# Optimization experiments

Hardware: AMD Instinct MI355X
Metric: run time of the kernel (lower is better)

Reference implementation:

```python
import jax, jax.numpy as jnp
import numpy as np

B, T, DM, H, DK, N_STEPS = 4, 1024, 1024, 16, 64, 3


def setup_inputs() -> dict:
    key = jax.random.key(0)
    ks = jax.random.split(key, 8)
    s = 1.0 / np.sqrt(DM).astype(np.float32)
    x = jax.random.normal(ks[0], (B, T, DM), jnp.float32)
    W_Q = jax.random.normal(ks[1], (DM, DM), jnp.float32) * s
    W_K = jax.random.normal(ks[2], (DM, DM), jnp.float32) * s
    W_re = jax.random.normal(ks[3], (DM, DM), jnp.float32) * s
    W_im = jax.random.normal(ks[4], (DM, DM), jnp.float32) * s
    W_V = jax.random.normal(ks[5], (DM, DM), jnp.float32) * s
    W_O = jax.random.normal(ks[6], (DM, DM), jnp.float32) * s
    logit_lam = jnp.float32(0.0)  # sigmoid(0)=0.5 == cfg.lam
    return {"x": x, "W_Q": W_Q, "W_K": W_K, "W_re": W_re, "W_im": W_im,
            "W_V": W_V, "W_O": W_O, "logit_lam": logit_lam}


def _heads(y):
    # (B,T,DM) -> (B,H,T,DK)
    return y.reshape(B, T, H, DK).transpose(0, 2, 1, 3)


def reference(x, W_Q, W_K, W_re, W_im, W_V, W_O, logit_lam):
    # AdjacencyBuilder: soft row-normalized adjacency
    Q = _heads(x @ W_Q)
    K = _heads(x @ W_K)
    scores = jnp.einsum('bhtd,bhsd->bhts', Q, K) / jnp.float32(np.sqrt(DK))
    A = jax.nn.softmax(scores, axis=-1)                      # (B,H,T,T)
    # PhaseEncoding: complex oscillator versors
    D = jax.lax.complex(_heads(x @ W_re), _heads(x @ W_im))  # (B,H,T,DK) c64
    # TopologyPropagation: D <- (1-lam) D + lam A D, n_steps times
    lam = jax.nn.sigmoid(logit_lam)
    A_c = A.astype(jnp.complex64)
    for _ in range(N_STEPS):
        D = (1.0 - lam) * D + lam * jnp.einsum('bhts,bhsd->bhtd', A_c, D)
    # CollapseReadout (phase_align): softmax over T of cosine to mean field
    mean_D = jnp.mean(D, axis=-2, keepdims=True)             # (B,H,1,DK)
    dot = (D * jnp.conj(mean_D)).real
    norm = jnp.abs(D) * jnp.abs(mean_D) + 1e-8
    gate = jax.nn.softmax(dot / norm, axis=-2)               # (B,H,T,DK)
    # Value gating + output projection (dropout is identity in eval)
    V = _heads(x @ W_V)
    out = (gate * V).transpose(0, 2, 1, 3).reshape(B, T, DM) @ W_O
    return out, gate
```

## Files before the change

kernel.cpp:

```cpp
#include <hip/hip_runtime.h>
#include <math.h>

#define Bc 4
#define Tc 1024
#define DMc 1024
#define Hc 16
#define DKc 64
#define BHc 64
#define Mc 4096
#define TD (Tc*DKc)
#define TD2 (Tc*128)
#define TDS (128*2048)

typedef __bf16 bf16_t;
typedef bf16_t bf16x4 __attribute__((ext_vector_type(4)));
typedef bf16_t bf16x8 __attribute__((ext_vector_type(8)));
typedef float  f32x4  __attribute__((ext_vector_type(4)));

#define KLSTR 136
#define DLSTR 72

__device__ __forceinline__ bf16x8 ld8(const bf16_t* p) {
    return *(const bf16x8*)p;
}
__device__ __forceinline__ void packsplit4(bf16_t* dh, bf16_t* dl, float4 v) {
    bf16x4 h, l;
    h[0]=(bf16_t)v.x; l[0]=(bf16_t)(v.x-(float)h[0]);
    h[1]=(bf16_t)v.y; l[1]=(bf16_t)(v.y-(float)h[1]);
    h[2]=(bf16_t)v.z; l[2]=(bf16_t)(v.z-(float)h[2]);
    h[3]=(bf16_t)v.w; l[3]=(bf16_t)(v.w-(float)h[3]);
    *(bf16x4*)dh = h; *(bf16x4*)dl = l;
}
__device__ __forceinline__ unsigned pk2(bf16_t a, bf16_t b) {
    unsigned short ua = __builtin_bit_cast(unsigned short, a);
    unsigned short ub = __builtin_bit_cast(unsigned short, b);
    return (unsigned)ua | ((unsigned)ub << 16);
}
__device__ __forceinline__ void gload16(const bf16_t* g, bf16_t* l) {
    __builtin_amdgcn_global_load_lds(
        (__attribute__((address_space(1))) void*)(bf16_t*)g,
        (__attribute__((address_space(3))) void*)l, 16, 0, 0);
}

__global__ __launch_bounds__(256)
void convx_k(const float* __restrict__ x,
             bf16_t* __restrict__ xh, bf16_t* __restrict__ xl)
{
    size_t i = ((size_t)blockIdx.x * 256 + threadIdx.x) * 4;
    float4 v = *(const float4*)&x[i];
    packsplit4(&xh[i], &xl[i], v);
}

__global__ __launch_bounds__(256)
void convw_k(const float* __restrict__ W0, const float* __restrict__ W1,
             const float* __restrict__ W2, const float* __restrict__ W3,
             const float* __restrict__ W4, const float* __restrict__ W5,
             bf16_t* __restrict__ WT)
{
    __shared__ float tile[32][33];
    const float* Ws[6] = {W0, W1, W2, W3, W4, W5};
    const int wi = blockIdx.z;
    const float* W = Ws[wi];
    bf16_t* WTh = WT + (size_t)wi * 2097152;
    bf16_t* WTl = WTh + 1048576;

    const int tx = threadIdx.x & 31, ty = threadIdx.x >> 5;
    const int k0 = blockIdx.x * 32, n0 = blockIdx.y * 32;
#pragma unroll
    for (int i = 0; i < 4; i++)
        tile[ty + 8*i][tx] = W[(size_t)(k0 + ty + 8*i) * DMc + n0 + tx];
    __syncthreads();
    const int kg = threadIdx.x & 7, n = threadIdx.x >> 3;
    float4 v = make_float4(tile[kg*4+0][n], tile[kg*4+1][n],
                           tile[kg*4+2][n], tile[kg*4+3][n]);
    const size_t o = (size_t)(n0 + n) * DMc + k0 + kg*4;
    packsplit4(&WTh[o], &WTl[o], v);
}

template<int MODE>
__global__ __launch_bounds__(256)
void mgemm_k(const bf16_t* __restrict__ Ah, const bf16_t* __restrict__ Al,
             const bf16_t* __restrict__ WT,
             bf16_t* __restrict__ Oq, bf16_t* __restrict__ Ok,
             bf16_t* __restrict__ Od, float* __restrict__ Ov,
             float* __restrict__ Of)
{
    __shared__ bf16_t S[4][128*32];

    const int tid = threadIdx.x;
    const int wv  = tid >> 6;
    const int ln  = tid & 63;
    const int l15 = ln & 15;
    const int qd  = ln >> 4;
    const int m0  = blockIdx.x * 128;
    const int by  = blockIdx.y;

    const bf16_t *Bh, *Bl;
    int n0, sel, kt0, kt1;
    float* Opart;
    if (MODE == 0) {
        sel = by >> 3;
        n0 = (by & 7) * 128;
        Bh = WT + (size_t)sel * 2097152;
        Bl = Bh + 1048576;
        kt0 = 0; kt1 = DMc;
        Opart = nullptr;
    } else {
        sel = 5;
        Bh = WT + (size_t)5 * 2097152;
        Bl = Bh + 1048576;
        n0 = by * 128;
        kt0 = blockIdx.z * 512; kt1 = kt0 + 512;
        Opart = Of + (size_t)blockIdx.z * ((size_t)Mc * DMc);
    }

    const int srow = ln >> 2;
    const int scol = (ln & 3) * 8;
    const bf16_t* sbase;
    if (wv == 0)      sbase = Ah + (size_t)(m0 + srow) * DMc + scol;
    else if (wv == 1) sbase = Al + (size_t)(m0 + srow) * DMc + scol;
    else if (wv == 2) sbase = Bh + (size_t)(n0 + srow) * DMc + scol;
    else              sbase = Bl + (size_t)(n0 + srow) * DMc + scol;
    sbase += kt0;
    bf16_t* ldst = &S[wv][0];

    f32x4 acc[4][4];
#pragma unroll
    for (int i = 0; i < 4; i++)
#pragma unroll
        for (int j = 0; j < 4; j++) acc[i][j] = (f32x4)0.f;

#pragma unroll 1
    for (int kt = kt0; kt < kt1; kt += 32) {
        __syncthreads();
#pragma unroll
        for (int i = 0; i < 8; i++)
            gload16(sbase + (size_t)i * 16 * DMc, ldst + i * 512);
        sbase += 32;
        __syncthreads();

        bf16x8 fah[4], fal[4], fbh[4], fbl[4];
#pragma unroll
        for (int it = 0; it < 4; it++) {
            const int row = ((wv>>1)*64 + it*16 + l15) * 32 + qd*8;
            fah[it] = *(const bf16x8*)&S[0][row];
            fal[it] = *(const bf16x8*)&S[1][row];
        }
#pragma unroll
        for (int jt = 0; jt < 4; jt++) {
            const int row = ((wv&1)*64 + jt*16 + l15) * 32 + qd*8;
            fbh[jt] = *(const bf16x8*)&S[2][row];
            fbl[jt] = *(const bf16x8*)&S[3][row];
        }
#pragma unroll
        for (int it = 0; it < 4; it++)
#pragma unroll
            for (int jt = 0; jt < 4; jt++) {
                acc[it][jt] = __builtin_amdgcn_mfma_f32_16x16x32_bf16(
                    fah[it], fbh[jt], acc[it][jt], 0, 0, 0);
                acc[it][jt] = __builtin_amdgcn_mfma_f32_16x16x32_bf16(
                    fah[it], fbl[jt], acc[it][jt], 0, 0, 0);
                acc[it][jt] = __builtin_amdgcn_mfma_f32_16x16x32_bf16(
                    fal[it], fbh[jt], acc[it][jt], 0, 0, 0);
            }
    }

#pragma unroll
    for (int it = 0; it < 4; it++) {
        const int mb = m0 + (wv>>1)*64 + it*16 + qd*4;
#pragma unroll
        for (int jt = 0; jt < 4; jt++) {
            const int col = n0 + (wv&1)*64 + jt*16 + l15;
            if (MODE == 0) {
                const int hh = col >> 6;
                const int b  = mb >> 10, t0 = mb & 1023;
                if (sel <= 1) {
                    bf16_t* O = sel ? Ok : Oq;
                    const int d = col & 63;
#pragma unroll
                    for (int r = 0; r < 4; r++) {
                        const float val = acc[it][jt][r];
                        const size_t o = ((size_t)(b*Hc + hh)*Tc + t0 + r)*128 + d;
                        bf16_t vh = (bf16_t)val;
                        O[o]      = vh;
                        O[o + 64] = (bf16_t)(val - (float)vh);
                    }
                } else if (sel <= 3) {
                    const int d = (sel == 3 ? 64 : 0) + (col & 63);
                    bf16x4 h4, l4;
#pragma unroll
                    for (int r = 0; r < 4; r++) {
                        const float val = acc[it][jt][r];
                        h4[r] = (bf16_t)val;
                        l4[r] = (bf16_t)(val - (float)h4[r]);
                    }
                    const size_t o = (size_t)(b*Hc + hh)*TDS + (size_t)d*2048 + t0;
                    *(bf16x4*)&Od[o]        = h4;
                    *(bf16x4*)&Od[o + 1024] = l4;
                } else {
#pragma unroll
                    for (int r = 0; r < 4; r++)
                        Ov[((size_t)(b*Hc + hh)*Tc + t0 + r)*64 + (col & 63)]
                            = acc[it][jt][r];
                }
            } else {
#pragma unroll
                for (int r = 0; r < 4; r++)
                    Opart[(size_t)(mb + r) * DMc + col] = acc[it][jt][r];
            }
        }
    }
}

__global__ __launch_bounds__(256)
void reduce2_k(const float* __restrict__ p0, const float* __restrict__ p1,
               float* __restrict__ out)
{
    size_t i = ((size_t)blockIdx.x * 256 + threadIdx.x) * 4;
    float4 a = *(const float4*)&p0[i];
    float4 b = *(const float4*)&p1[i];
    *(float4*)&out[i] = make_float4(a.x+b.x, a.y+b.y, a.z+b.z, a.w+b.w);
}

template<int FINAL>
__global__ __launch_bounds__(256)
void prop_k(const bf16_t* __restrict__ Qg, const bf16_t* __restrict__ Kg,
            const bf16_t* __restrict__ DTin, bf16_t* __restrict__ DTout,
            float* __restrict__ Dc, const float* __restrict__ llam)
{
    __shared__ bf16_t Ks[32*KLSTR];
    __shared__ bf16_t Ds[128*DLSTR];

    const int tid = threadIdx.x;
    const int wv  = tid >> 6;
    const int ln  = tid & 63;
    const int l15 = ln & 15;
    const int qd  = ln >> 4;
    const int bh  = blockIdx.x;
    const int Tw  = blockIdx.y * 128 + wv * 32;

    const bf16_t* Qh  = Qg   + (size_t)bh * (Tc*128);
    const bf16_t* Kh  = Kg   + (size_t)bh * (Tc*128);
    const bf16_t* DTh = DTin + (size_t)bh * TDS;

    bf16x8 qfh[2][2], qfl[2][2];
#pragma unroll
    for (int tj = 0; tj < 2; tj++) {
        const bf16_t* qp = &Qh[(size_t)(Tw + tj*16 + l15) * 128];
#pragma unroll
        for (int ks = 0; ks < 2; ks++) {
            qfh[tj][ks] = *(const bf16x8*)&qp[ks*32 + qd*8];
            qfl[tj][ks] = *(const bf16x8*)&qp[64 + ks*32 + qd*8];
        }
    }

    const int idk0 = tid, idk1 = tid + 256;
    const bf16_t* srcK0 = Kh + (size_t)(idk0 >> 4) * 128 + (idk0 & 15) * 8;
    const bf16_t* srcK1 = Kh + (size_t)(idk1 >> 4) * 128 + (idk1 & 15) * 8;
    bf16_t* dstK0 = &Ks[(idk0 >> 4) * KLSTR + (idk0 & 15) * 8];
    bf16_t* dstK1 = &Ks[(idk1 >> 4) * KLSTR + (idk1 & 15) * 8];
    const bf16_t* srcD[4];
    bf16_t* dstD[4];
#pragma unroll
    for (int i = 0; i < 4; i++) {
        const int id = tid + i * 256;
        const int r = id >> 3, sg = id & 7;
        srcD[i] = DTh + (size_t)r * 2048
                      + (sg < 4 ? sg * 8 : 1024 + (sg - 4) * 8);
        dstD[i] = (sg < 4) ? &Ds[r * DLSTR + sg * 8]
                           : &Ds[r * DLSTR + 32 + (sg - 4) * 8];
    }
    bf16x8 kr0 = *(const bf16x8*)srcK0;
    bf16x8 kr1 = *(const bf16x8*)srcK1;
    bf16x8 dr[4];
#pragma unroll
    for (int i = 0; i < 4; i++) dr[i] = *(const bf16x8*)srcD[i];

    f32x4 acc[8][2];
#pragma unroll
    for (int i = 0; i < 8; i++)
#pragma unroll
        for (int j = 0; j < 2; j++) acc[i][j] = (f32x4)0.f;
    float rs[2] = {0.f, 0.f};

    const int srcA = (((qd & 1) * 2)     << 4) | l15;
    const int srcB = (((qd & 1) * 2 + 1) << 4) | l15;
    const bool loQuad = (qd < 2);

#pragma unroll 1
    for (int ch = 0; ch < 32; ch++) {
        __syncthreads();
        *(bf16x8*)dstK0 = kr0;
        *(bf16x8*)dstK1 = kr1;
#pragma unroll
        for (int i = 0; i < 4; i++) *(bf16x8*)dstD[i] = dr[i];
        __syncthreads();
        if (ch < 31) {
            kr0 = *(const bf16x8*)(srcK0 + (size_t)(ch + 1) * 4096);
            kr1 = *(const bf16x8*)(srcK1 + (size_t)(ch + 1) * 4096);
#pragma unroll
            for (int i = 0; i < 4; i++)
                dr[i] = *(const bf16x8*)(srcD[i] + (size_t)(ch + 1) * 32);
        }
        bf16x8 kfh[2][2], kfl[2][2];
#pragma unroll
        for (int si = 0; si < 2; si++) {
            const int row = (si*16 + l15) * KLSTR;
#pragma unroll
            for (int ks = 0; ks < 2; ks++) {
                kfh[si][ks] = ld8(&Ks[row + ks*32 + qd*8]);
                kfl[si][ks] = ld8(&Ks[row + 64 + ks*32 + qd*8]);
            }
        }
        f32x4 pacc[2][2];
#pragma unroll
        for (int si = 0; si < 2; si++)
#pragma unroll
            for (int tj = 0; tj < 2; tj++) pacc[si][tj] = (f32x4)0.f;
#pragma unroll
        for (int ks = 0; ks < 2; ks++)
#pragma unroll
            for (int si = 0; si < 2; si++)
#pragma unroll
                for (int tj = 0; tj < 2; tj++) {
                    pacc[si][tj] = __builtin_amdgcn_mfma_f32_16x16x32_bf16(
                        kfh[si][ks], qfh[tj][ks], pacc[si][tj], 0, 0, 0);
                    pacc[si][tj] = __builtin_amdgcn_mfma_f32_16x16x32_bf16(
                        kfl[si][ks], qfh[tj][ks], pacc[si][tj], 0, 0, 0);
                    pacc[si][tj] = __builtin_amdgcn_mfma_f32_16x16x32_bf16(
                        kfh[si][ks], qfl[tj][ks], pacc[si][tj], 0, 0, 0);
                }
        unsigned pk01h[2][2], pk23h[2][2], pk01l[2][2], pk23l[2][2];
#pragma unroll
        for (int si = 0; si < 2; si++)
#pragma unroll
            for (int tj = 0; tj < 2; tj++) {
                float e0 = __expf(pacc[si][tj][0] * 0.125f);
                float e1 = __expf(pacc[si][tj][1] * 0.125f);
                float e2 = __expf(pacc[si][tj][2] * 0.125f);
                float e3 = __expf(pacc[si][tj][3] * 0.125f);
                rs[tj] += (e0 + e1) + (e2 + e3);
                bf16_t h0=(bf16_t)e0, h1=(bf16_t)e1, h2=(bf16_t)e2, h3=(bf16_t)e3;
                pk01h[si][tj] = pk2(h0, h1);
                pk23h[si][tj] = pk2(h2, h3);
                pk01l[si][tj] = pk2((bf16_t)(e0-(float)h0), (bf16_t)(e1-(float)h1));
                pk23l[si][tj] = pk2((bf16_t)(e2-(float)h2), (bf16_t)(e3-(float)h3));
            }
        bf16x8 pfh[2], pfl[2];
#pragma unroll
        for (int tj = 0; tj < 2; tj++) {
            union { bf16x8 v; unsigned u[4]; } H, L;
            unsigned a0 = __shfl((int)pk01h[0][tj], srcA, 64);
            unsigned a1 = __shfl((int)pk23h[0][tj], srcA, 64);
            unsigned a2 = __shfl((int)pk01h[0][tj], srcB, 64);
            unsigned a3 = __shfl((int)pk23h[0][tj], srcB, 64);
            unsigned b0 = __shfl((int)pk01h[1][tj], srcA, 64);
            unsigned b1 = __shfl((int)pk23h[1][tj], srcA, 64);
            unsigned b2 = __shfl((int)pk01h[1][tj], srcB, 64);
            unsigned b3 = __shfl((int)pk23h[1][tj], srcB, 64);
            H.u[0] = loQuad ? a0 : b0;  H.u[1] = loQuad ? a1 : b1;
            H.u[2] = loQuad ? a2 : b2;  H.u[3] = loQuad ? a3 : b3;
            unsigned c0 = __shfl((int)pk01l[0][tj], srcA, 64);
            unsigned c1 = __shfl((int)pk23l[0][tj], srcA, 64);
            unsigned c2 = __shfl((int)pk01l[0][tj], srcB, 64);
            unsigned c3 = __shfl((int)pk23l[0][tj], srcB, 64);
            unsigned d0_ = __shfl((int)pk01l[1][tj], srcA, 64);
            unsigned d1 = __shfl((int)pk23l[1][tj], srcA, 64);
            unsigned d2 = __shfl((int)pk01l[1][tj], srcB, 64);
            unsigned d3 = __shfl((int)pk23l[1][tj], srcB, 64);
            L.u[0] = loQuad ? c0 : d0_; L.u[1] = loQuad ? c1 : d1;
            L.u[2] = loQuad ? c2 : d2;  L.u[3] = loQuad ? c3 : d3;
            pfh[tj] = H.v; pfl[tj] = L.v;
        }
#pragma unroll
        for (int half = 0; half < 2; half++) {
            bf16x8 dfh[4], dfl[4];
#pragma unroll
            for (int i = 0; i < 4; i++) {
                const int row = ((half*4 + i)*16 + l15) * DLSTR;
                dfh[i] = ld8(&Ds[row + qd*8]);
                dfl[i] = ld8(&Ds[row + 32 + qd*8]);
            }
#pragma unroll
            for (int i = 0; i < 4; i++)
#pragma unroll
                for (int tj = 0; tj < 2; tj++) {
                    acc[half*4+i][tj] = __builtin_amdgcn_mfma_f32_16x16x32_bf16(
                        dfh[i], pfh[tj], acc[half*4+i][tj], 0, 0, 0);
                    acc[half*4+i][tj] = __builtin_amdgcn_mfma_f32_16x16x32_bf16(
                        dfh[i], pfl[tj], acc[half*4+i][tj], 0, 0, 0);
                    acc[half*4+i][tj] = __builtin_amdgcn_mfma_f32_16x16x32_bf16(
                        dfl[i], pfh[tj], acc[half*4+i][tj], 0, 0, 0);
                }
        }
    }

#pragma unroll
    for (int tj = 0; tj < 2; tj++) {
        rs[tj] += __shfl_xor(rs[tj], 16);
        rs[tj] += __shfl_xor(rs[tj], 32);
    }

    const float lam = 1.f / (1.f + __expf(-llam[0]));
    const float oml = 1.f - lam;
    bf16_t* DToutg = (FINAL ? (bf16_t*)nullptr : DTout + (size_t)bh * TDS);

#pragma unroll
    for (int tj = 0; tj < 2; tj++) {
        const int t = Tw + tj*16 + l15;
        const float s = lam / rs[tj];
#pragma unroll
        for (int it = 0; it < 8; it++) {
            const int d0 = it*16 + qd*4;
            float v[4];
#pragma unroll
            for (int r = 0; r < 4; r++) {
                const size_t ro = (size_t)(d0 + r)*2048 + t;
                float res = (float)DTh[ro] + (float)DTh[ro + 1024];
                v[r] = oml*res + s*acc[it][tj][r];
            }
            if (FINAL) {
                *(float4*)&Dc[((size_t)bh*Tc + t)*128 + d0] =
                    make_float4(v[0], v[1], v[2], v[3]);
            } else {
#pragma unroll
                for (int r = 0; r < 4; r++) {
                    const size_t ro = (size_t)(d0 + r)*2048 + t;
                    bf16_t h = (bf16_t)v[r];
                    DToutg[ro]        = h;
                    DToutg[ro + 1024] = (bf16_t)(v[r] - (float)h);
                }
            }
        }
    }
}

__global__ __launch_bounds__(256)
void mean1_k(const float* __restrict__ D,
             float* __restrict__ M1re, float* __restrict__ M1im)
{
    __shared__ float sre[4][64], sim[4][64];
    const int bh = blockIdx.x, y = blockIdx.y;
    const int d = threadIdx.x & 63, q = threadIdx.x >> 6;
    const float* p = D + (size_t)bh * TD2;
    float ar = 0.f, ai = 0.f;
    const int t0 = y*128 + q*32;
    for (int t = t0; t < t0 + 32; t++) {
        ar += p[t*128 + d]; ai += p[t*128 + 64 + d];
    }
    sre[q][d] = ar; sim[q][d] = ai;
    __syncthreads();
    if (threadIdx.x < 64) {
        M1re[(bh*8 + y)*64 + d] = sre[0][d]+sre[1][d]+sre[2][d]+sre[3][d];
        M1im[(bh*8 + y)*64 + d] = sim[0][d]+sim[1][d]+sim[2][d]+sim[3][d];
    }
}

__global__ __launch_bounds__(64)
void mean2_k(const float* __restrict__ M1re, const float* __restrict__ M1im,
             float* __restrict__ Mre, float* __restrict__ Mim)
{
    const int bh = blockIdx.x, d = threadIdx.x;
    float r = 0.f, im = 0.f;
    for (int y = 0; y < 8; y++) {
        r  += M1re[(bh*8 + y)*64 + d];
        im += M1im[(bh*8 + y)*64 + d];
    }
    Mre[bh*64 + d] = r  * (1.f/1024.f);
    Mim[bh*64 + d] = im * (1.f/1024.f);
}

__global__ __launch_bounds__(256)
void gate1_k(const float* __restrict__ D,
             const float* __restrict__ Mre, const float* __restrict__ Mim,
             float* __restrict__ Gp)
{
    __shared__ float part[4][64];
    const int bh = blockIdx.x, y = blockIdx.y;
    const int d = threadIdx.x & 63, q = threadIdx.x >> 6;
    const float* p = D + (size_t)bh * TD2;
    const float mre = Mre[bh*64 + d], mim = Mim[bh*64 + d];
    const float mabs = sqrtf(mre*mre + mim*mim);

    float ps = 0.f;
    const int t0 = y*128 + q*32;
    for (int t = t0; t < t0 + 32; t++) {
        float dr = p[t*128 + d], dv = p[t*128 + 64 + d];
        float c = (dr*mre + dv*mim) / (sqrtf(dr*dr + dv*dv)*mabs + 1e-8f);
        ps += __expf(c);
    }
    part[q][d] = ps;
    __syncthreads();
    if (threadIdx.x < 64)
        Gp[(bh*8 + y)*64 + d] = part[0][d]+part[1][d]+part[2][d]+part[3][d];
}

__global__ __launch_bounds__(256)
void gate2_k(const float* __restrict__ D,
             const float* __restrict__ Mre, const float* __restrict__ Mim,
             const float* __restrict__ V, const float* __restrict__ Gp,
             float* __restrict__ gate_out,
             bf16_t* __restrict__ gVh, bf16_t* __restrict__ gVl)
{
    __shared__ float dinv[64];
    const int bh = blockIdx.x, y = blockIdx.y;
    const int d = threadIdx.x & 63, q = threadIdx.x >> 6;
    if (threadIdx.x < 64) {
        float s = 0.f;
        for (int yy = 0; yy < 8; yy++) s += Gp[(bh*8 + yy)*64 + d];
        dinv[d] = 1.f / s;
    }
    __syncthreads();

    const float* p = D + (size_t)bh * TD2;
    const float mre = Mre[bh*64 + d], mim = Mim[bh*64 + d];
    const float mabs = sqrtf(mre*mre + mim*mim);
    const float di_ = dinv[d];
    const int b = bh >> 4, hh = bh & 15;
    const float* pv = V + (size_t)bh * TD;
    const int t0 = y*128 + q*32;
    for (int t = t0; t < t0 + 32; t++) {
        float dr = p[t*128 + d], dv = p[t*128 + 64 + d];
        float c = (dr*mre + dv*mim) / (sqrtf(dr*dr + dv*dv)*mabs + 1e-8f);
        float g = __expf(c) * di_;
        gate_out[(size_t)bh*TD + t*64 + d] = g;
        float gv = g * pv[t*64 + d];
        size_t o = ((size_t)b*Tc + t)*DMc + hh*64 + d;
        bf16_t gh = (bf16_t)gv;
        gVh[o] = gh;
        gVl[o] = (bf16_t)(gv - (float)gh);
    }
}

extern "C" void kernel_launch(void* const* d_in, const int* in_sizes, int n_in,
                              void* d_out, int out_size, void* d_ws, size_t ws_size,
                              hipStream_t stream)
{
    const float* x    = (const float*)d_in[0];
    const float* W_Q  = (const float*)d_in[1];
    const float* W_K  = (const float*)d_in[2];
    const float* W_re = (const float*)d_in[3];
    const float* W_im = (const float*)d_in[4];
    const float* W_V  = (const float*)d_in[5];
    const float* W_O  = (const float*)d_in[6];
    const float* llam = (const float*)d_in[7];

    float* out      = (float*)d_out;
    float* gate_out = out + (size_t)Mc * DMc;

    float* ws = (float*)d_ws;
    const size_t M1 = 1024*1024;
    float*  Dc  = ws;
    bf16_t* DT1 = (bf16_t*)ws;
    bf16_t* DT0 = (bf16_t*)(ws + 8*M1);
    float*  V   = ws + 16*M1;
    bf16_t* Qs  = (bf16_t*)(ws + 20*M1);
    bf16_t* Ksb = (bf16_t*)(ws + 24*M1);
    float*  Mre = ws + 28*M1;
    float*  Mim = Mre + 4096;
    bf16_t* xh  = (bf16_t*)(ws + 28*M1 + 8192);
    bf16_t* xl  = xh + 4*M1;
    bf16_t* WT  = xl + 4*M1;
    bf16_t* gVh = xh;
    bf16_t* gVl = xl;
    float* Gp   = ws + 24*M1;
    float* M1re = Gp + 32768;
    float* M1im = M1re + 32768;
    float* P0 = ws + 8*M1;
    float* P1 = ws + 12*M1;

    convx_k<<<4096, 256, 0, stream>>>(x, xh, xl);
    convw_k<<<dim3(32, 32, 6), 256, 0, stream>>>(
        W_Q, W_K, W_re, W_im, W_V, W_O, WT);

    mgemm_k<0><<<dim3(32, 40), 256, 0, stream>>>(
        xh, xl, WT, Qs, Ksb, DT0, V, nullptr);

    prop_k<0><<<dim3(64, 8), 256, 0, stream>>>(Qs, Ksb, DT0, DT1, nullptr, llam);
    prop_k<0><<<dim3(64, 8), 256, 0, stream>>>(Qs, Ksb, DT1, DT0, nullptr, llam);
    prop_k<1><<<dim3(64, 8), 256, 0, stream>>>(Qs, Ksb, DT0, nullptr, Dc, llam);

    mean1_k<<<dim3(64, 8), 256, 0, stream>>>(Dc, M1re, M1im);
    mean2_k<<<64, 64, 0, stream>>>(M1re, M1im, Mre, Mim);
    gate1_k<<<dim3(64, 8), 256, 0, stream>>>(Dc, Mre, Mim, Gp);
    gate2_k<<<dim3(64, 8), 256, 0, stream>>>(Dc, Mre, Mim, V, Gp,
                                             gate_out, gVh, gVl);

    mgemm_k<1><<<dim3(32, 8, 2), 256, 0, stream>>>(
        gVh, gVl, WT, nullptr, nullptr, nullptr, nullptr, P0);
    reduce2_k<<<4096, 256, 0, stream>>>(P0, P1, out);
}
```

Baseline: 606.2 us.

## Pair projection weights per block to reuse loaded x tiles across two outputs

In the input projection GEMM, each block now computes two weight matrices (Q/K and re/im) against the same x tile. The A tile is staged once into shared memory and reused for both, with twice the accumulators, and the grid shrinks from 40 to 24 column groups. The intent is to cut redundant global loads of x and raise MFMA work per load. In exchange it uses more shared memory and registers, and the launch bounds are changed to request two blocks per CU, which may cause spills or leave some blocks (V) doing half the work.

New measurement: 581.3 us, median of 2. 4.1% less time.

```diff
diff --git a/kernel.cpp b/kernel.cpp
--- a/kernel.cpp
+++ b/kernel.cpp
@@ -78,14 +78,14 @@
 }
 
 template<int MODE>
-__global__ __launch_bounds__(256)
+__global__ __launch_bounds__(256, 2)
 void mgemm_k(const bf16_t* __restrict__ Ah, const bf16_t* __restrict__ Al,
              const bf16_t* __restrict__ WT,
              bf16_t* __restrict__ Oq, bf16_t* __restrict__ Ok,
              bf16_t* __restrict__ Od, float* __restrict__ Ov,
              float* __restrict__ Of)
 {
-    __shared__ bf16_t S[4][128*32];
+    __shared__ bf16_t S[6][128*32];
 
     const int tid = threadIdx.x;
     const int wv  = tid >> 6;
@@ -95,118 +95,185 @@
     const int m0  = blockIdx.x * 128;
     const int by  = blockIdx.y;
 
-    const bf16_t *Bh, *Bl;
-    int n0, sel, kt0, kt1;
+    int n0, sel0, kt0, kt1;
+    bool two;
     float* Opart;
     if (MODE == 0) {
-        sel = by >> 3;
+        const int pi = by >> 3;
+        sel0 = pi * 2;
+        two  = (pi < 2);
         n0 = (by & 7) * 128;
-        Bh = WT + (size_t)sel * 2097152;
-        Bl = Bh + 1048576;
         kt0 = 0; kt1 = DMc;
         Opart = nullptr;
     } else {
-        sel = 5;
-        Bh = WT + (size_t)5 * 2097152;
-        Bl = Bh + 1048576;
+        sel0 = 5;
+        two  = false;
         n0 = by * 128;
         kt0 = blockIdx.z * 512; kt1 = kt0 + 512;
         Opart = Of + (size_t)blockIdx.z * ((size_t)Mc * DMc);
     }
+    const bf16_t* B0h = WT + (size_t)sel0 * 2097152;
+    const bf16_t* B0l = B0h + 1048576;
+    const bf16_t* B1h = B0h + 2097152;
+    const bf16_t* B1l = B1h + 1048576;
 
     const int srow = ln >> 2;
     const int scol = (ln & 3) * 8;
-    const bf16_t* sbase;
-    if (wv == 0)      sbase = Ah + (size_t)(m0 + srow) * DMc + scol;
-    else if (wv == 1) sbase = Al + (size_t)(m0 + srow) * DMc + scol;
-    else if (wv == 2) sbase = Bh + (size_t)(n0 + srow) * DMc + scol;
-    else              sbase = Bl + (size_t)(n0 + srow) * DMc + scol;
-    sbase += kt0;
-    bf16_t* ldst = &S[wv][0];
-
-    f32x4 acc[4][4];
+    const bf16_t* gAh = Ah  + (size_t)(m0 + srow) * DMc + scol + kt0;
+    const bf16_t* gAl = Al  + (size_t)(m0 + srow) * DMc + scol + kt0;
+    const bf16_t* gB0h = B0h + (size_t)(n0 + srow) * DMc + scol + kt0;
+    const bf16_t* gB0l = B0l + (size_t)(n0 + srow) * DMc + scol + kt0;
+    const bf16_t* gB1h = B1h + (size_t)(n0 + srow) * DMc + scol + kt0;
+    const bf16_t* gB1l = B1l + (size_t)(n0 + srow) * DMc + scol + kt0;
+
+    f32x4 acc[2][4][4];
+#pragma unroll
+    for (int p = 0; p < 2; p++)
 #pragma unroll
     for (int i = 0; i < 4; i++)
 #pragma unroll
-        for (int j = 0; j < 4; j++) acc[i][j] = (f32x4)0.f;
+        for (int j = 0; j < 4; j++) acc[p][i][j] = (f32x4)0.f;
 
 #pragma unroll 1
     for (int kt = kt0; kt < kt1; kt += 32) {
         __syncthreads();
-#pragma unroll
-        for (int i = 0; i < 8; i++)
-            gload16(sbase + (size_t)i * 16 * DMc, ldst + i * 512);
-        sbase += 32;
+        if (two) {
+            if (wv == 0) {
+#pragma unroll
+                for (int i = 0; i < 8; i++)
+                    gload16(gAh + (size_t)i * 16 * DMc, &S[0][i * 512]);
+#pragma unroll
+                for (int i = 0; i < 4; i++)
+                    gload16(gAl + (size_t)i * 16 * DMc, &S[1][i * 512]);
+            } else if (wv == 1) {
+#pragma unroll
+                for (int i = 4; i < 8; i++)
+                    gload16(gAl + (size_t)i * 16 * DMc, &S[1][i * 512]);
+#pragma unroll
+                for (int i = 0; i < 8; i++)
+                    gload16(gB0h + (size_t)i * 16 * DMc, &S[2][i * 512]);
+            } else if (wv == 2) {
+#pragma unroll
+                for (int i = 0; i < 8; i++)
+                    gload16(gB0l + (size_t)i * 16 * DMc, &S[3][i * 512]);
+#pragma unroll
+                for (int i = 0; i < 4; i++)
+                    gload16(gB1h + (size_t)i * 16 * DMc, &S[4][i * 512]);
+            } else {
+#pragma unroll
+                for (int i = 4; i < 8; i++)
+                    gload16(gB1h + (size_t)i * 16 * DMc, &S[4][i * 512]);
+#pragma unroll
+                for (int i = 0; i < 8; i++)
+                    gload16(gB1l + (size_t)i * 16 * DMc, &S[5][i * 512]);
+            }
+        } else {
+            const bf16_t* sb = (wv == 0) ? gAh : (wv == 1) ? gAl
+                              : (wv == 2) ? gB0h : gB0l;
+            bf16_t* ld = &S[wv][0];
+#pragma unroll
+            for (int i = 0; i < 8; i++)
+                gload16(sb + (size_t)i * 16 * DMc, ld + i * 512);
+        }
+        gAh += 32; gAl += 32; gB0h += 32; gB0l += 32; gB1h += 32; gB1l += 32;
         __syncthreads();
 
-        bf16x8 fah[4], fal[4], fbh[4], fbl[4];
+        bf16x8 fah[4], fal[4];
 #pragma unroll
         for (int it = 0; it < 4; it++) {
             const int row = ((wv>>1)*64 + it*16 + l15) * 32 + qd*8;
             fah[it] = *(const bf16x8*)&S[0][row];
             fal[it] = *(const bf16x8*)&S[1][row];
         }
-#pragma unroll
-        for (int jt = 0; jt < 4; jt++) {
-            const int row = ((wv&1)*64 + jt*16 + l15) * 32 + qd*8;
-            fbh[jt] = *(const bf16x8*)&S[2][row];
-            fbl[jt] = *(const bf16x8*)&S[3][row];
-        }
-#pragma unroll
-        for (int it = 0; it < 4; it++)
+        {
+            bf16x8 fbh[4], fbl[4];
 #pragma unroll
             for (int jt = 0; jt < 4; jt++) {
-                acc[it][jt] = __builtin_amdgcn_mfma_f32_16x16x32_bf16(
-                    fah[it], fbh[jt], acc[it][jt], 0, 0, 0);
-                acc[it][jt] = __builtin_amdgcn_mfma_f32_16x16x32_bf16(
-                    fah[it], fbl[jt], acc[it][jt], 0, 0, 0);
-                acc[it][jt] = __builtin_amdgcn_mfma_f32_16x16x32_bf16(
-                    fal[it], fbh[jt], acc[it][jt], 0, 0, 0);
-            }
-    }
-
-#pragma unroll
-    for (int it = 0; it < 4; it++) {
-        const int mb = m0 + (wv>>1)*64 + it*16 + qd*4;
-#pragma unroll
-        for (int jt = 0; jt < 4; jt++) {
-            const int col = n0 + (wv&1)*64 + jt*16 + l15;
-            if (MODE == 0) {
-                const int hh = col >> 6;
-                const int b  = mb >> 10, t0 = mb & 1023;
-                if (sel <= 1) {
-                    bf16_t* O = sel ? Ok : Oq;
-                    const int d = col & 63;
-#pragma unroll
-                    for (int r = 0; r < 4; r++) {
-                        const float val = acc[it][jt][r];
-                        const size_t o = ((size_t)(b*Hc + hh)*Tc + t0 + r)*128 + d;
-                        bf16_t vh = (bf16_t)val;
-                        O[o]      = vh;
-                        O[o + 64] = (bf16_t)(val - (float)vh);
+                const int row = ((wv&1)*64 + jt*16 + l15) * 32 + qd*8;
+                fbh[jt] = *(const bf16x8*)&S[2][row];
+                fbl[jt] = *(const bf16x8*)&S[3][row];
+            }
+#pragma unroll
+            for (int it = 0; it < 4; it++)
+#pragma unroll
+                for (int jt = 0; jt < 4; jt++) {
+                    acc[0][it][jt] = __builtin_amdgcn_mfma_f32_16x16x32_bf16(
+                        fah[it], fbh[jt], acc[0][it][jt], 0, 0, 0);
+                    acc[0][it][jt] = __builtin_amdgcn_mfma_f32_16x16x32_bf16(
+                        fah[it], fbl[jt], acc[0][it][jt], 0, 0, 0);
+                    acc[0][it][jt] = __builtin_amdgcn_mfma_f32_16x16x32_bf16(
+                        fal[it], fbh[jt], acc[0][it][jt], 0, 0, 0);
+                }
+        }
+        if (two) {
+            bf16x8 fbh[4], fbl[4];
+#pragma unroll
+            for (int jt = 0; jt < 4; jt++) {
+                const int row = ((wv&1)*64 + jt*16 + l15) * 32 + qd*8;
+                fbh[jt] = *(const bf16x8*)&S[4][row];
+                fbl[jt] = *(const bf16x8*)&S[5][row];
+            }
+#pragma unroll
+            for (int it = 0; it < 4; it++)
+#pragma unroll
+                for (int jt = 0; jt < 4; jt++) {
+                    acc[1][it][jt] = __builtin_amdgcn_mfma_f32_16x16x32_bf16(
+                        fah[it], fbh[jt], acc[1][it][jt], 0, 0, 0);
+                    acc[1][it][jt] = __builtin_amdgcn_mfma_f32_16x16x32_bf16(
+                        fah[it], fbl[jt], acc[1][it][jt], 0, 0, 0);
+                    acc[1][it][jt] = __builtin_amdgcn_mfma_f32_16x16x32_bf16(
+                        fal[it], fbh[jt], acc[1][it][jt], 0, 0, 0);
+                }
+        }
+    }
+
+#pragma unroll
+    for (int p = 0; p < 2; p++) {
+        if (p == 1 && !two) continue;
+        const int sel = (MODE == 0) ? sel0 + p : 5;
+#pragma unroll
+        for (int it = 0; it < 4; it++) {
+            const int mb = m0 + (wv>>1)*64 + it*16 + qd*4;
+#pragma unroll
+            for (int jt = 0; jt < 4; jt++) {
+                const int col = n0 + (wv&1)*64 + jt*16 + l15;
+                if (MODE == 0) {
+                    const int hh = col >> 6;
+                    const int b  = mb >> 10, t0 = mb & 1023;
+                    if (sel <= 1) {
+                        bf16_t* O = sel ? Ok : Oq;
+                        const int d = col & 63;
+#pragma unroll
+                        for (int r = 0; r < 4; r++) {
+                            const float val = acc[p][it][jt][r];
+                            const size_t o = ((size_t)(b*Hc + hh)*Tc + t0 + r)*128 + d;
+                            bf16_t vh = (bf16_t)val;
+                            O[o]      = vh;
+                            O[o + 64] = (bf16_t)(val - (float)vh);
+                        }
+                    } else if (sel <= 3) {
+                        const int d = (sel == 3 ? 64 : 0) + (col & 63);
+                        bf16x4 h4, l4;
+#pragma unroll
+                        for (int r = 0; r < 4; r++) {
+                            const float val = acc[p][it][jt][r];
+                            h4[r] = (bf16_t)val;
+                            l4[r] = (bf16_t)(val - (float)h4[r]);
+                        }
+                        const size_t o = (size_t)(b*Hc + hh)*TDS + (size_t)d*2048 + t0;
+                        *(bf16x4*)&Od[o]        = h4;
+                        *(bf16x4*)&Od[o + 1024] = l4;
+                    } else {
+#pragma unroll
+                        for (int r = 0; r < 4; r++)
+                            Ov[((size_t)(b*Hc + hh)*Tc + t0 + r)*64 + (col & 63)]
+                                = acc[p][it][jt][r];
                     }
-                } else if (sel <= 3) {
-                    const int d = (sel == 3 ? 64 : 0) + (col & 63);
-                    bf16x4 h4, l4;
-#pragma unroll
-                    for (int r = 0; r < 4; r++) {
-                        const float val = acc[it][jt][r];
-                        h4[r] = (bf16_t)val;
-                        l4[r] = (bf16_t)(val - (float)h4[r]);
-                    }
-                    const size_t o = (size_t)(b*Hc + hh)*TDS + (size_t)d*2048 + t0;
-                    *(bf16x4*)&Od[o]        = h4;
-                    *(bf16x4*)&Od[o + 1024] = l4;
                 } else {
 #pragma unroll
                     for (int r = 0; r < 4; r++)
-                        Ov[((size_t)(b*Hc + hh)*Tc + t0 + r)*64 + (col & 63)]
-                            = acc[it][jt][r];
+                        Opart[(size_t)(mb + r) * DMc + col] = acc[p][it][jt][r];
                 }
-            } else {
-#pragma unroll
-                for (int r = 0; r < 4; r++)
-                    Opart[(size_t)(mb + r) * DMc + col] = acc[it][jt][r];
             }
         }
     }
@@ -573,7 +640,7 @@
     convw_k<<<dim3(32, 32, 6), 256, 0, stream>>>(
         W_Q, W_K, W_re, W_im, W_V, W_O, WT);
 
-    mgemm_k<0><<<dim3(32, 40), 256, 0, stream>>>(
+    mgemm_k<0><<<dim3(32, 24), 256, 0, stream>>>(
         xh, xl, WT, Qs, Ksb, DT0, V, nullptr);
 
     prop_k<0><<<dim3(64, 8), 256, 0, stream>>>(Qs, Ksb, DT0, DT1, nullptr, llam);
```
